# Kernel tuning notes

Measured on AMD Instinct MI355X. Metric: run time of the kernel, lower is better.

Reference implementation:

```python
import jax, jax.numpy as jnp
import numpy as np

N = 50000      # nodes
E = 800000     # edges (avg degree 16)
F_IN = 128     # num_features
H = 128        # hidden_channels
C = 64         # num_classes
K = 3          # TAGConv hops (PyG default)


def setup_inputs() -> dict:
    key = jax.random.key(0)
    k0, k1, k2, k3 = jax.random.split(key, 4)
    x = jax.random.normal(k0, (N, F_IN), dtype=jnp.float32)
    edge_index = jax.random.randint(k1, (2, E), 0, N, dtype=jnp.int32)
    W1 = jax.random.normal(k2, (K + 1, F_IN, H), dtype=jnp.float32) / np.sqrt(F_IN).astype(np.float32)
    b1 = jnp.zeros((H,), dtype=jnp.float32)
    W2 = jax.random.normal(k3, (K + 1, H, C), dtype=jnp.float32) / np.sqrt(H).astype(np.float32)
    b2 = jnp.zeros((C,), dtype=jnp.float32)
    return {"x": x, "edge_index": edge_index, "W1": W1, "b1": b1, "W2": W2, "b2": b2}


def _gcn_norm(row, col):
    # PyG gcn_norm with add_self_loops=False (TAGConv default):
    # deg over target nodes (col), norm = d^-1/2[row] * d^-1/2[col]
    deg = jax.ops.segment_sum(jnp.ones((E,), dtype=jnp.float32), col, num_segments=N)
    dinv = jnp.where(deg > 0, jax.lax.rsqrt(jnp.maximum(deg, 1.0)) * jnp.where(deg > 0, 1.0, 0.0), 0.0)
    dinv = jnp.where(deg > 0, deg ** -0.5, 0.0)
    return dinv[row] * dinv[col]


def _tag_conv(h, row, col, norm, W, b):
    # out = sum_{k=0..K} A_hat^k h @ W[k] + b, A_hat = D^-1/2 A D^-1/2
    out = h @ W[0]
    for k in range(1, K + 1):
        h = jax.ops.segment_sum(norm[:, None] * h[row], col, num_segments=N)  # [N, d]
        out = out + h @ W[k]
    return out + b


def reference(x, edge_index, W1, b1, W2, b2):
    row, col = edge_index[0], edge_index[1]
    norm = _gcn_norm(row, col)  # [E]
    h = jax.nn.relu(_tag_conv(x, row, col, norm, W1, b1))
    # F.dropout with training=False is the identity (inference reference)
    out = _tag_conv(h, row, col, norm, W2, b2)
    return jax.nn.log_softmax(out, axis=1)
```

## Files before the change

### kernel.cpp

```cpp
#include <hip/hip_runtime.h>
#include <stdint.h>

#define NN 50000
#define EE 800000
#define NROWS 50048
#define CB 196
#define CAP 5120
#define ACH 4096

typedef unsigned int u32;
typedef unsigned short u16;
using f32x4 = __attribute__((ext_vector_type(4))) float;
using short8 = __attribute__((ext_vector_type(8))) short;

__device__ __forceinline__ float bflo(u32 u) { return __uint_as_float(u << 16); }
__device__ __forceinline__ float bfhi(u32 u) { return __uint_as_float(u & 0xFFFF0000u); }
__device__ __forceinline__ float bf1(u16 v) { return __uint_as_float(((u32)v) << 16); }
__device__ __forceinline__ u32 f2bf(float f) {
    u32 u = __float_as_uint(f);
    return (u + 0x7FFFu + ((u >> 16) & 1u)) >> 16;
}
__device__ __forceinline__ u32 pack2(float lo, float hi) {
    return f2bf(lo) | (f2bf(hi) << 16);
}

__device__ __forceinline__ int excl_scan256(int v, int tid) {
    __shared__ int ws_[4];
    int lane = tid & 63, w = tid >> 6;
    int x = v;
    #pragma unroll
    for (int off = 1; off < 64; off <<= 1) {
        int y = __shfl_up(x, off, 64);
        if (lane >= off) x += y;
    }
    if (lane == 63) ws_[w] = x;
    __syncthreads();
    int add = 0;
    if (w > 0) add += ws_[0];
    if (w > 1) add += ws_[1];
    if (w > 2) add += ws_[2];
    return add + x - v;
}


__global__ void detect_kernel(const u32* __restrict__ xw, int* __restrict__ flag) {
    int tid = threadIdx.x;
    int cnt = 0;
    for (int i = tid; i < 8192; i += 256) {
        u32 u = xw[i];
        int e0 = (u >> 7) & 0xFF, e1 = (u >> 23) & 0xFF;
        cnt += (e0 >= 0xC3) + (e1 >= 0xC3);
    }
    #pragma unroll
    for (int off = 32; off; off >>= 1) cnt += __shfl_xor(cnt, off, 64);
    __shared__ int wsum[4];
    if ((tid & 63) == 0) wsum[tid >> 6] = cnt;
    __syncthreads();
    if (tid == 0) flag[0] = (wsum[0] + wsum[1] + wsum[2] + wsum[3] > 100) ? 1 : 0;
}


__global__ __launch_bounds__(256) void phaseA_kernel(const int* __restrict__ ei,
                                                     int* __restrict__ ccnt,
                                                     u32* __restrict__ cpad) {
    __shared__ int hist[256], lstart[256], lofs[256], gbase[256];
    __shared__ u32 srt[ACH];
    int tid = threadIdx.x;
    int e0 = blockIdx.x * ACH;
    int nv = EE - e0; if (nv > ACH) nv = ACH;
    hist[tid] = 0;
    __syncthreads();
    u32 pk[16];
    int bn[16];
    #pragma unroll
    for (int i = 0; i < 16; i++) {
        int e = e0 + tid + i * 256;
        bn[i] = -1;
        if (e < EE) {
            int r = ei[e], c = ei[EE + e];
            bn[i] = c >> 8;
            pk[i] = (u32)r | ((u32)(c & 255) << 16) | ((u32)bn[i] << 24);
            atomicAdd(&hist[bn[i]], 1);
        }
    }
    __syncthreads();
    int v = hist[tid];
    int excl = excl_scan256(v, tid);
    lstart[tid] = excl;
    lofs[tid] = excl;
    gbase[tid] = atomicAdd(&ccnt[tid], v);
    __syncthreads();
    #pragma unroll
    for (int i = 0; i < 16; i++)
        if (bn[i] >= 0) {
            int lp = atomicAdd(&lofs[bn[i]], 1);
            srt[lp] = pk[i];
        }
    __syncthreads();
    for (int j = tid; j < nv; j += 256) {
        u32 pv = srt[j];
        int b = pv >> 24;
        cpad[(size_t)b * CAP + gbase[b] + (j - lstart[b])] = pv;
    }
}

__global__ void cscan_kernel(const int* __restrict__ ccnt, int* __restrict__ cbase,
                             int* __restrict__ rowptr, float* __restrict__ dinv) {
    int tid = threadIdx.x;
    int v = ccnt[tid];
    int excl = excl_scan256(v, tid);
    cbase[tid] = excl;
    if (tid == 0) {
        rowptr[NN] = EE;
        rowptr[NN + 1] = EE;
        dinv[NN] = 0.f;
    }
}


__global__ __launch_bounds__(256) void phaseB_kernel(const u32* __restrict__ cpad,
                                                     const int* __restrict__ ccnt,
                                                     const int* __restrict__ cbase,
                                                     u16* __restrict__ esrc,
                                                     int* __restrict__ rowptr,
                                                     float* __restrict__ dinv,
                                                     float* __restrict__ rinv) {
    __shared__ int hist[256], lstart[256], lofs[256];
    __shared__ u16 srt[CAP];
    int tid = threadIdx.x, cb = blockIdx.x;
    int cnt = ccnt[cb], base = cbase[cb];
    hist[tid] = 0;
    __syncthreads();
    for (int j = tid; j < cnt; j += 256)
        atomicAdd(&hist[(cpad[(size_t)cb * CAP + j] >> 16) & 255], 1);
    __syncthreads();
    int v = hist[tid];
    int excl = excl_scan256(v, tid);
    lstart[tid] = excl;
    lofs[tid] = excl;
    int g = cb * 256 + tid;
    if (g < NN) {
        rowptr[g] = base + excl;
        dinv[g] = v > 0 ? rsqrtf((float)v) : 0.f;
        rinv[g] = v > 0 ? sqrtf((float)v) : 0.f;
    }
    __syncthreads();
    for (int j = tid; j < cnt; j += 256) {
        u32 pv = cpad[(size_t)cb * CAP + j];
        int lp = atomicAdd(&lofs[(pv >> 16) & 255], 1);
        srt[lp] = (u16)(pv & 0xFFFF);
    }
    __syncthreads();
    for (int j = tid; j < cnt; j += 256) esrc[base + j] = srt[j];
}

__global__ void wprep_kernel(const void* __restrict__ w, u16* __restrict__ wt,
                             int fout, int nk, int mode, int total,
                             const int* __restrict__ flag) {
    int idx = blockIdx.x * 256 + threadIdx.x;
    if (idx >= total) return;
    u16 v = flag[0] ? (u16)f2bf(((const float*)w)[idx]) : ((const u16*)w)[idx];
    int per = 128 * fout;
    int k = idx / per, rem = idx % per;
    int in = rem / fout, o = rem % fout;
    size_t J;
    if (mode == 0) J = (size_t)(k * 16 + (in >> 3)) * fout + o;
    else J = (size_t)(in >> 3) * (nk * fout) + k * fout + o;
    wt[J * 8 + (in & 7)] = v;
}

__global__ void bprep_kernel(const void* __restrict__ b1, const void* __restrict__ b2,
                             float* __restrict__ bf, const int* __restrict__ flag) {
    int i = threadIdx.x;
    if (i < 128) bf[i] = flag[0] ? ((const float*)b1)[i] : bf1(((const u16*)b1)[i]);
    else {
        int j = i - 128;
        bf[i] = flag[0] ? ((const float*)b2)[j] : bf1(((const u16*)b2)[j]);
    }
}


__global__ void scalex_kernel(const void* __restrict__ x, u32* __restrict__ g0,
                              u32* __restrict__ xb, const float* __restrict__ dinv,
                              const int* __restrict__ flag) {
    int i = blockIdx.x * 256 + threadIdx.x;
    if (i >= (NN + 1) * 64) return;
    int node = i >> 6;
    int fl = flag[0];
    if (node == NN) {
        g0[i] = 0;
        if (fl) xb[i] = 0;
        return;
    }
    float dv = dinv[node];
    float a, b;
    if (fl) {
        const float* xf = (const float*)x;
        a = xf[2 * i];
        b = xf[2 * i + 1];
        xb[i] = pack2(a, b);
    } else {
        u32 u = ((const u32*)x)[i];
        a = bflo(u);
        b = bfhi(u);
    }
    g0[i] = pack2(a * dv, b * dv);
}


__global__ __launch_bounds__(256) void propg_kernel(const u32* __restrict__ gin,
                                                    u32* __restrict__ gout,
                                                    const int* __restrict__ rowptr,
                                                    const u16* __restrict__ esrc,
                                                    const float* __restrict__ dinv) {
    int node = (blockIdx.x * 256 + threadIdx.x) >> 6;
    int lane = threadIdx.x & 63;
    if (node > NN) return;
    int e0 = rowptr[node], e1 = rowptr[node + 1];
    float ax = 0.f, ay = 0.f;
    for (int base = e0; base < e1; base += 64) {
        int s_l = NN;
        if (base + lane < e1) s_l = esrc[base + lane];
        int cnt = e1 - base;
        if (cnt > 64) cnt = 64;
        for (int j = 0; j < cnt; j += 16) {
            u32 hv[16];
            #pragma unroll
            for (int u = 0; u < 16; u++) {
                int s = __builtin_amdgcn_readlane(s_l, j + u);
                hv[u] = gin[(size_t)s * 64 + lane];
            }
            #pragma unroll
            for (int u = 0; u < 16; u++) {
                ax += bflo(hv[u]);
                ay += bfhi(hv[u]);
            }
        }
    }
    float d = dinv[node];
    float d2 = d * d;
    gout[(size_t)node * 64 + lane] = pack2(ax * d2, ay * d2);
}


__device__ __forceinline__ float gatheru(const u16* __restrict__ uin, int e0, int e1,
                                         int lane, const u16* __restrict__ esrc) {
    float a = 0.f;
    for (int base = e0; base < e1; base += 64) {
        int s_l = NN;
        if (base + lane < e1) s_l = esrc[base + lane];
        int cnt = e1 - base;
        if (cnt > 64) cnt = 64;
        for (int j = 0; j < cnt; j += 16) {
            float hv[16];
            #pragma unroll
            for (int u = 0; u < 16; u++) {
                int s = __builtin_amdgcn_readlane(s_l, j + u);
                hv[u] = bf1(uin[(size_t)s * 64 + lane]);
            }
            #pragma unroll
            for (int u = 0; u < 16; u++) a += hv[u];
        }
    }
    return a;
}

__global__ __launch_bounds__(256) void prop64_add_kernel(const u16* __restrict__ uin,
                                                         const u16* __restrict__ zadd,
                                                         u16* __restrict__ uout,
                                                         const int* __restrict__ rowptr,
                                                         const u16* __restrict__ esrc,
                                                         const float* __restrict__ dinv) {
    int node = (blockIdx.x * 256 + threadIdx.x) >> 6;
    int lane = threadIdx.x & 63;
    if (node > NN) return;
    float s = gatheru(uin, rowptr[node], rowptr[node + 1], lane, esrc);
    float d = dinv[node];
    float r = fmaf(d * d, s, d * bf1(zadd[(size_t)node * 64 + lane]));
    uout[(size_t)node * 64 + lane] = (u16)f2bf(r);
}

__global__ __launch_bounds__(256) void prop64_final_kernel(const u16* __restrict__ uin,
                                                           const u16* __restrict__ z0,
                                                           const float* __restrict__ bias,
                                                           void* __restrict__ outv,
                                                           const int* __restrict__ rowptr,
                                                           const u16* __restrict__ esrc,
                                                           const float* __restrict__ dinv,
                                                           const int* __restrict__ flag) {
    int node = (blockIdx.x * 256 + threadIdx.x) >> 6;
    int lane = threadIdx.x & 63;
    if (node >= NN) return;
    float sg = gatheru(uin, rowptr[node], rowptr[node + 1], lane, esrc);
    float v = dinv[node] * sg + bf1(z0[(size_t)node * 64 + lane]) + bias[lane];
    float m = v;
    #pragma unroll
    for (int off = 32; off; off >>= 1) m = fmaxf(m, __shfl_xor(m, off, 64));
    float e = __expf(v - m);
    float s = e;
    #pragma unroll
    for (int off = 32; off; off >>= 1) s += __shfl_xor(s, off, 64);
    float r = v - m - __logf(s);
    if (flag[0]) ((float*)outv)[(size_t)node * 64 + lane] = r;
    else ((u16*)outv)[(size_t)node * 64 + lane] = (u16)f2bf(r);
}


__device__ __forceinline__ short8 ld8(const u16* p) {
    return __builtin_bit_cast(short8, *(const uint4*)p);
}

template <int NT>
__global__ __launch_bounds__(256) void gemm1_kernel(const u32* __restrict__ a0,
                                                    const u32* __restrict__ a0alt,
                                                    const u32* __restrict__ a1,
                                                    const u32* __restrict__ a2,
                                                    const u32* __restrict__ a3,
                                                    const u16* __restrict__ wt,
                                                    const float* __restrict__ rinv,
                                                    const float* __restrict__ bias,
                                                    u32* __restrict__ outH,
                                                    const int* __restrict__ flag) {
    __shared__ uint4 hs[1024];
    const u32* A0 = flag[0] ? a0alt : a0;
    const u32* bufs[4] = {A0, a1, a2, a3};
    int t = threadIdx.x;
    int lane = t & 63, w = t >> 6;
    int row0 = blockIdx.x * 64;
    int cb = (NT == 4) ? (int)blockIdx.y * 64 : 0;
    int m = lane & 15, qo = lane >> 4;
    f32x4 accx[NT], accg[NT];
    #pragma unroll
    for (int tt = 0; tt < NT; tt++) {
        accx[tt] = (f32x4){0.f, 0.f, 0.f, 0.f};
        accg[tt] = (f32x4){0.f, 0.f, 0.f, 0.f};
    }

    uint4 p[4];
    {
        const uint4* src = (const uint4*)A0 + (size_t)row0 * 16;
        #pragma unroll
        for (int i = 0; i < 4; i++) p[i] = src[t + 256 * i];
    }
    #pragma unroll
    for (int hop = 0; hop < 4; hop++) {
        __syncthreads();
        #pragma unroll
        for (int i = 0; i < 4; i++) {
            int g = t + 256 * i;
            hs[(g >> 4) * 16 + ((g & 15) ^ ((g >> 4) & 15))] = p[i];
        }
        __syncthreads();
        if (hop + 1 < 4) {
            const uint4* src = (const uint4*)bufs[hop + 1] + (size_t)row0 * 16;
            #pragma unroll
            for (int i = 0; i < 4; i++) p[i] = src[t + 256 * i];
        }
        #pragma unroll
        for (int q = 0; q < 4; q++) {
            short8 a = __builtin_bit_cast(short8,
                hs[(16 * w + m) * 16 + ((q * 4 + qo) ^ m)]);
            short8 b[NT];
            #pragma unroll
            for (int tt = 0; tt < NT; tt++)
                b[tt] = ld8(wt + ((size_t)(hop * 16 + q * 4 + qo) * 128 + cb + 16 * tt + m) * 8);
            if (hop == 0) {
                #pragma unroll
                for (int tt = 0; tt < NT; tt++)
                    accx[tt] = __builtin_amdgcn_mfma_f32_16x16x32_bf16(a, b[tt], accx[tt], 0, 0, 0);
            } else {
                #pragma unroll
                for (int tt = 0; tt < NT; tt++)
                    accg[tt] = __builtin_amdgcn_mfma_f32_16x16x32_bf16(a, b[tt], accg[tt], 0, 0, 0);
            }
        }
    }

    int r0 = row0 + 16 * w + qo * 4;
    float rv[4];
    #pragma unroll
    for (int r = 0; r < 4; r++) rv[r] = (r0 + r < NN) ? rinv[r0 + r] : 0.f;
    __syncthreads();
    u16* lds16 = (u16*)hs;
    #pragma unroll
    for (int tt = 0; tt < NT; tt++) {
        float bs = bias[cb + 16 * tt + m];
        #pragma unroll
        for (int r = 0; r < 4; r++) {
            int rr = r0 + r;
            float vv = 0.f;
            if (rr < NN) vv = fmaxf(accx[tt][r] + rv[r] * accg[tt][r] + bs, 0.f);
            lds16[(16 * w + qo * 4 + r) * (16 * NT) + 16 * tt + m] = (u16)f2bf(vv);
        }
    }
    __syncthreads();
    uint4* out4 = (uint4*)outH;
    const uint4* epi4 = (const uint4*)hs;
    if (NT == 8) {
        #pragma unroll
        for (int i = 0; i < 4; i++) {
            int g = t + 256 * i;
            int row = g >> 4, ch = g & 15;
            out4[(size_t)(row0 + row) * 16 + ch] = epi4[g];
        }
    } else {
        #pragma unroll
        for (int i = 0; i < 2; i++) {
            int g = t + 256 * i;
            int row = g >> 3, ch = g & 7;
            out4[(size_t)(row0 + row) * 16 + (cb >> 3) + ch] = epi4[g];
        }
    }
}

__global__ __launch_bounds__(256) void gemmz_kernel(const u32* __restrict__ aH,
                                                    const u16* __restrict__ wt,
                                                    const float* __restrict__ dinv,
                                                    u16* __restrict__ p0, u16* __restrict__ p1,
                                                    u16* __restrict__ p2, u16* __restrict__ p3) {
    __shared__ uint4 hs[1024];
    int t = threadIdx.x;
    int lane = t & 63, w = t >> 6;
    int row0 = blockIdx.x * 64;
    int py = blockIdx.y;
    int cb = py * 64;
    int m = lane & 15, qo = lane >> 4;
    f32x4 acc[4];
    #pragma unroll
    for (int tt = 0; tt < 4; tt++) acc[tt] = (f32x4){0.f, 0.f, 0.f, 0.f};
    {
        const uint4* src = (const uint4*)aH + (size_t)row0 * 16;
        #pragma unroll
        for (int i = 0; i < 4; i++) {
            int g = t + 256 * i;
            hs[(g >> 4) * 16 + ((g & 15) ^ ((g >> 4) & 15))] = src[g];
        }
    }
    __syncthreads();
    #pragma unroll
    for (int q = 0; q < 4; q++) {
        short8 a = __builtin_bit_cast(short8,
            hs[(16 * w + m) * 16 + ((q * 4 + qo) ^ m)]);
        short8 b[4];
        #pragma unroll
        for (int tt = 0; tt < 4; tt++)
            b[tt] = ld8(wt + ((size_t)(q * 4 + qo) * 256 + cb + 16 * tt + m) * 8);
        #pragma unroll
        for (int tt = 0; tt < 4; tt++)
            acc[tt] = __builtin_amdgcn_mfma_f32_16x16x32_bf16(a, b[tt], acc[tt], 0, 0, 0);
    }
    u16* zp = (py == 0) ? p0 : (py == 1) ? p1 : (py == 2) ? p2 : p3;
    int r0 = row0 + 16 * w + qo * 4;
    float sc[4];
    #pragma unroll
    for (int r = 0; r < 4; r++) {
        int rr = r0 + r;
        sc[r] = (rr < NN) ? ((py == 3) ? dinv[rr] : 1.f) : 0.f;
    }
    __syncthreads();
    u16* lds16 = (u16*)hs;
    #pragma unroll
    for (int tt = 0; tt < 4; tt++) {
        #pragma unroll
        for (int r = 0; r < 4; r++) {
            lds16[(16 * w + qo * 4 + r) * 64 + 16 * tt + m] = (u16)f2bf(sc[r] * acc[tt][r]);
        }
    }
    __syncthreads();
    uint4* zp4 = (uint4*)zp;
    const uint4* epi4 = (const uint4*)hs;
    #pragma unroll
    for (int i = 0; i < 2; i++) {
        int g = t + 256 * i;
        int row = g >> 3, ch = g & 7;
        zp4[(size_t)(row0 + row) * 8 + ch] = epi4[g];
    }
}


extern "C" void kernel_launch(void* const* d_in, const int* in_sizes, int n_in,
                              void* d_out, int out_size, void* d_ws, size_t ws_size,
                              hipStream_t stream) {
    const void* x  = d_in[0];
    const int*  ei = (const int*)d_in[1];
    const void* W1 = d_in[2];
    const void* b1 = d_in[3];
    const void* W2 = d_in[4];
    const void* b2 = d_in[5];

    char* ws = (char*)d_ws;
    size_t p = 0;
    auto alloc = [&](size_t bytes) -> void* {
        void* r = ws + p;
        p = (p + bytes + 255) & ~(size_t)255;
        return r;
    };
    int*   flag   = (int*)  alloc(256);
    int*   rowptr = (int*)  alloc((size_t)(NN + 2) * 4);
    float* dinv   = (float*)alloc((size_t)(NN + 64) * 4);
    float* rinv   = (float*)alloc((size_t)(NN + 64) * 4);
    int*   ccnt   = (int*)  alloc(256 * 4);
    int*   cbase  = (int*)  alloc(256 * 4);
    u16*   esrc   = (u16*)  alloc((size_t)EE * 2);
    u16*   wt1    = (u16*)  alloc((size_t)64 * 128 * 16);
    u16*   wt2    = (u16*)  alloc((size_t)16 * 256 * 16);
    float* biasF  = (float*)alloc(192 * 4);
    const size_t hbytes = (size_t)(NROWS + 16) * 64 * 4;
    u32* X = (u32*)alloc(hbytes);
    u32* P = (u32*)alloc(hbytes);
    u32* Q = (u32*)alloc(hbytes);
    u32* R = (u32*)alloc(hbytes);
    int cs = (p + hbytes + 256 <= ws_size) ? 1 : 0;
    u32* H5 = cs ? (u32*)alloc(hbytes) : Q;
    u32* cpad = X;

    const size_t ZP = (size_t)(NROWS + 16) * 64;
    u16* zR0 = (u16*)R;
    u16* zR1 = (u16*)R + ZP;
    u16* zP0 = (u16*)P;
    u16* zP1 = (u16*)P + ZP;
    u16* uX0 = (u16*)X;

    hipMemsetAsync(ccnt, 0, 256 * 4, stream);
    detect_kernel<<<1, 256, 0, stream>>>((const u32*)x, flag);
    phaseA_kernel<<<(EE + ACH - 1) / ACH, 256, 0, stream>>>(ei, ccnt, cpad);
    cscan_kernel<<<1, 256, 0, stream>>>(ccnt, cbase, rowptr, dinv);
    phaseB_kernel<<<CB, 256, 0, stream>>>(cpad, ccnt, cbase, esrc, rowptr, dinv, rinv);
    wprep_kernel<<<(4 * 128 * 128 + 255) / 256, 256, 0, stream>>>(
        W1, wt1, 128, 4, 0, 4 * 128 * 128, flag);
    wprep_kernel<<<(4 * 128 * 64 + 255) / 256, 256, 0, stream>>>(
        W2, wt2, 64, 4, 1, 4 * 128 * 64, flag);
    bprep_kernel<<<1, 192, 0, stream>>>(b1, b2, biasF, flag);

    const int PGX = ((NN + 1) * 64 + 255) / 256;
    const int PGF = (NN * 64) / 256;
    const int GG = NROWS / 64;

    scalex_kernel<<<PGX, 256, 0, stream>>>(x, P, X, dinv, flag);

    propg_kernel<<<PGX, 256, 0, stream>>>(P, Q, rowptr, esrc, dinv);
    propg_kernel<<<PGX, 256, 0, stream>>>(Q, R, rowptr, esrc, dinv);
    propg_kernel<<<PGX, 256, 0, stream>>>(R, P, rowptr, esrc, dinv);
    if (cs)
        gemm1_kernel<4><<<dim3(GG, 2), 256, 0, stream>>>(
            (const u32*)x, X, Q, R, P, wt1, rinv, biasF, H5, flag);
    else
        gemm1_kernel<8><<<GG, 256, 0, stream>>>(
            (const u32*)x, X, Q, R, P, wt1, rinv, biasF, Q, flag);

    gemmz_kernel<<<dim3(GG, 4), 256, 0, stream>>>(H5, wt2, dinv, zR0, zR1, zP0, zP1);
    prop64_add_kernel<<<PGX, 256, 0, stream>>>(zP1, zP0, uX0, rowptr, esrc, dinv);
    prop64_add_kernel<<<PGX, 256, 0, stream>>>(uX0, zR1, zP0, rowptr, esrc, dinv);
    prop64_final_kernel<<<PGF, 256, 0, stream>>>(zP0, zR0, biasF + 128, d_out,
                                                 rowptr, esrc, dinv, flag);
}
```

Baseline: 342.2 us.

## Fuse layer-1 GEMM with layer-2 projection GEMM into one kernel

Adds gemm1z_kernel, which computes the layer-1 hidden tile (ReLU, bias and rinv scaling), keeps it in LDS, and immediately multiplies it by all four layer-2 weight slices. The four Z planes are written directly. This removes the separate gemmz launch and the global write and re-read of the hidden activations. In exchange it drops the 2-way column split of gemm1, giving fewer blocks and more accumulator registers per thread, which may lower occupancy. It also needs extra workspace for two buffers and falls back to the old path otherwise.

```diff
diff --git a/kernel.cpp b/kernel.cpp
--- a/kernel.cpp
+++ b/kernel.cpp
@@ -310,7 +310,140 @@
     return __builtin_bit_cast(short8, *(const uint4*)p);
 }
 
-template <int NT>
+__global__ __launch_bounds__(256) void gemm1z_kernel(const u32* __restrict__ a0,
+                                                     const u32* __restrict__ a0alt,
+                                                     const u32* __restrict__ a1,
+                                                     const u32* __restrict__ a2,
+                                                     const u32* __restrict__ a3,
+                                                     const u16* __restrict__ wt1,
+                                                     const u16* __restrict__ wt2,
+                                                     const float* __restrict__ rinv,
+                                                     const float* __restrict__ dinv,
+                                                     const float* __restrict__ bias,
+                                                     u16* __restrict__ p0, u16* __restrict__ p1,
+                                                     u16* __restrict__ p2, u16* __restrict__ p3,
+                                                     const int* __restrict__ flag) {
+    __shared__ uint4 hs[1024];
+    const u32* A0 = flag[0] ? a0alt : a0;
+    const u32* bufs[4] = {A0, a1, a2, a3};
+    int t = threadIdx.x;
+    int lane = t & 63, w = t >> 6;
+    int row0 = blockIdx.x * 64;
+    int m = lane & 15, qo = lane >> 4;
+    f32x4 accx[8], accg[8];
+    #pragma unroll
+    for (int tt = 0; tt < 8; tt++) {
+        accx[tt] = (f32x4){0.f, 0.f, 0.f, 0.f};
+        accg[tt] = (f32x4){0.f, 0.f, 0.f, 0.f};
+    }
+
+    uint4 p[4];
+    {
+        const uint4* src = (const uint4*)A0 + (size_t)row0 * 16;
+        #pragma unroll
+        for (int i = 0; i < 4; i++) p[i] = src[t + 256 * i];
+    }
+    #pragma unroll
+    for (int hop = 0; hop < 4; hop++) {
+        __syncthreads();
+        #pragma unroll
+        for (int i = 0; i < 4; i++) {
+            int g = t + 256 * i;
+            hs[(g >> 4) * 16 + ((g & 15) ^ ((g >> 4) & 15))] = p[i];
+        }
+        __syncthreads();
+        if (hop + 1 < 4) {
+            const uint4* src = (const uint4*)bufs[hop + 1] + (size_t)row0 * 16;
+            #pragma unroll
+            for (int i = 0; i < 4; i++) p[i] = src[t + 256 * i];
+        }
+        #pragma unroll
+        for (int q = 0; q < 4; q++) {
+            short8 a = __builtin_bit_cast(short8,
+                hs[(16 * w + m) * 16 + ((q * 4 + qo) ^ m)]);
+            short8 b[8];
+            #pragma unroll
+            for (int tt = 0; tt < 8; tt++)
+                b[tt] = ld8(wt1 + ((size_t)(hop * 16 + q * 4 + qo) * 128 + 16 * tt + m) * 8);
+            if (hop == 0) {
+                #pragma unroll
+                for (int tt = 0; tt < 8; tt++)
+                    accx[tt] = __builtin_amdgcn_mfma_f32_16x16x32_bf16(a, b[tt], accx[tt], 0, 0, 0);
+            } else {
+                #pragma unroll
+                for (int tt = 0; tt < 8; tt++)
+                    accg[tt] = __builtin_amdgcn_mfma_f32_16x16x32_bf16(a, b[tt], accg[tt], 0, 0, 0);
+            }
+        }
+    }
+
+    int r0 = row0 + 16 * w + qo * 4;
+    float rv[4], scp3[4];
+    #pragma unroll
+    for (int r = 0; r < 4; r++) {
+        int rr = r0 + r;
+        rv[r] = (rr < NN) ? rinv[rr] : 0.f;
+        scp3[r] = (rr < NN) ? dinv[rr] : 0.f;
+    }
+    __syncthreads();
+    u16* lds16 = (u16*)hs;
+    #pragma unroll
+    for (int tt = 0; tt < 8; tt++) {
+        float bs = bias[16 * tt + m];
+        #pragma unroll
+        for (int r = 0; r < 4; r++) {
+            int rr = r0 + r;
+            float vv = 0.f;
+            if (rr < NN) vv = fmaxf(accx[tt][r] + rv[r] * accg[tt][r] + bs, 0.f);
+            int lrow = 16 * w + qo * 4 + r;
+            int col = 16 * tt + m;
+            lds16[lrow * 128 + (((col >> 3) ^ (lrow & 15)) << 3) + (col & 7)] = (u16)f2bf(vv);
+        }
+    }
+    __syncthreads();
+    f32x4 az[4][4];
+    #pragma unroll
+    for (int py = 0; py < 4; py++)
+        #pragma unroll
+        for (int tt = 0; tt < 4; tt++) az[py][tt] = (f32x4){0.f, 0.f, 0.f, 0.f};
+    #pragma unroll
+    for (int q = 0; q < 4; q++) {
+        short8 a = __builtin_bit_cast(short8,
+            hs[(16 * w + m) * 16 + ((q * 4 + qo) ^ m)]);
+        #pragma unroll
+        for (int py = 0; py < 4; py++) {
+            #pragma unroll
+            for (int tt = 0; tt < 4; tt++) {
+                short8 b = ld8(wt2 + ((size_t)(q * 4 + qo) * 256 + py * 64 + 16 * tt + m) * 8);
+                az[py][tt] = __builtin_amdgcn_mfma_f32_16x16x32_bf16(a, b, az[py][tt], 0, 0, 0);
+            }
+        }
+    }
+    u16* planes[4] = {p0, p1, p2, p3};
+    #pragma unroll
+    for (int py = 0; py < 4; py++) {
+        __syncthreads();
+        #pragma unroll
+        for (int tt = 0; tt < 4; tt++) {
+            #pragma unroll
+            for (int r = 0; r < 4; r++) {
+                int rr = r0 + r;
+                float sc = (rr < NN) ? ((py == 3) ? scp3[r] : 1.f) : 0.f;
+                lds16[(16 * w + qo * 4 + r) * 64 + 16 * tt + m] = (u16)f2bf(sc * az[py][tt][r]);
+            }
+        }
+        __syncthreads();
+        uint4* zp4 = (uint4*)planes[py];
+        const uint4* epi4 = (const uint4*)hs;
+        #pragma unroll
+        for (int i = 0; i < 2; i++) {
+            int g = t + 256 * i;
+            int row = g >> 3, ch = g & 7;
+            zp4[(size_t)(row0 + row) * 8 + ch] = epi4[g];
+        }
+    }
+}
+
 __global__ __launch_bounds__(256) void gemm1_kernel(const u32* __restrict__ a0,
                                                     const u32* __restrict__ a0alt,
                                                     const u32* __restrict__ a1,
@@ -327,15 +460,13 @@
     int t = threadIdx.x;
     int lane = t & 63, w = t >> 6;
     int row0 = blockIdx.x * 64;
-    int cb = (NT == 4) ? (int)blockIdx.y * 64 : 0;
     int m = lane & 15, qo = lane >> 4;
-    f32x4 accx[NT], accg[NT];
-    #pragma unroll
-    for (int tt = 0; tt < NT; tt++) {
+    f32x4 accx[8], accg[8];
+    #pragma unroll
+    for (int tt = 0; tt < 8; tt++) {
         accx[tt] = (f32x4){0.f, 0.f, 0.f, 0.f};
         accg[tt] = (f32x4){0.f, 0.f, 0.f, 0.f};
     }
-
     uint4 p[4];
     {
         const uint4* src = (const uint4*)A0 + (size_t)row0 * 16;
@@ -360,22 +491,21 @@
         for (int q = 0; q < 4; q++) {
             short8 a = __builtin_bit_cast(short8,
                 hs[(16 * w + m) * 16 + ((q * 4 + qo) ^ m)]);
-            short8 b[NT];
-            #pragma unroll
-            for (int tt = 0; tt < NT; tt++)
-                b[tt] = ld8(wt + ((size_t)(hop * 16 + q * 4 + qo) * 128 + cb + 16 * tt + m) * 8);
+            short8 b[8];
+            #pragma unroll
+            for (int tt = 0; tt < 8; tt++)
+                b[tt] = ld8(wt + ((size_t)(hop * 16 + q * 4 + qo) * 128 + 16 * tt + m) * 8);
             if (hop == 0) {
                 #pragma unroll
-                for (int tt = 0; tt < NT; tt++)
+                for (int tt = 0; tt < 8; tt++)
                     accx[tt] = __builtin_amdgcn_mfma_f32_16x16x32_bf16(a, b[tt], accx[tt], 0, 0, 0);
             } else {
                 #pragma unroll
-                for (int tt = 0; tt < NT; tt++)
+                for (int tt = 0; tt < 8; tt++)
                     accg[tt] = __builtin_amdgcn_mfma_f32_16x16x32_bf16(a, b[tt], accg[tt], 0, 0, 0);
             }
         }
     }
-
     int r0 = row0 + 16 * w + qo * 4;
     float rv[4];
     #pragma unroll
@@ -383,33 +513,24 @@
     __syncthreads();
     u16* lds16 = (u16*)hs;
     #pragma unroll
-    for (int tt = 0; tt < NT; tt++) {
-        float bs = bias[cb + 16 * tt + m];
+    for (int tt = 0; tt < 8; tt++) {
+        float bs = bias[16 * tt + m];
         #pragma unroll
         for (int r = 0; r < 4; r++) {
             int rr = r0 + r;
             float vv = 0.f;
             if (rr < NN) vv = fmaxf(accx[tt][r] + rv[r] * accg[tt][r] + bs, 0.f);
-            lds16[(16 * w + qo * 4 + r) * (16 * NT) + 16 * tt + m] = (u16)f2bf(vv);
+            lds16[(16 * w + qo * 4 + r) * 128 + 16 * tt + m] = (u16)f2bf(vv);
         }
     }
     __syncthreads();
     uint4* out4 = (uint4*)outH;
     const uint4* epi4 = (const uint4*)hs;
-    if (NT == 8) {
-        #pragma unroll
-        for (int i = 0; i < 4; i++) {
-            int g = t + 256 * i;
-            int row = g >> 4, ch = g & 15;
-            out4[(size_t)(row0 + row) * 16 + ch] = epi4[g];
-        }
-    } else {
-        #pragma unroll
-        for (int i = 0; i < 2; i++) {
-            int g = t + 256 * i;
-            int row = g >> 3, ch = g & 7;
-            out4[(size_t)(row0 + row) * 16 + (cb >> 3) + ch] = epi4[g];
-        }
+    #pragma unroll
+    for (int i = 0; i < 4; i++) {
+        int g = t + 256 * i;
+        int row = g >> 4, ch = g & 15;
+        out4[(size_t)(row0 + row) * 16 + ch] = epi4[g];
     }
 }
 
@@ -510,16 +631,12 @@
     u32* P = (u32*)alloc(hbytes);
     u32* Q = (u32*)alloc(hbytes);
     u32* R = (u32*)alloc(hbytes);
-    int cs = (p + hbytes + 256 <= ws_size) ? 1 : 0;
-    u32* H5 = cs ? (u32*)alloc(hbytes) : Q;
+    int fused = (p + 2 * hbytes + 256 <= ws_size) ? 1 : 0;
+    u32* H5 = fused ? (u32*)alloc(hbytes) : nullptr;
+    u32* H6 = fused ? (u32*)alloc(hbytes) : nullptr;
     u32* cpad = X;
 
     const size_t ZP = (size_t)(NROWS + 16) * 64;
-    u16* zR0 = (u16*)R;
-    u16* zR1 = (u16*)R + ZP;
-    u16* zP0 = (u16*)P;
-    u16* zP1 = (u16*)P + ZP;
-    u16* uX0 = (u16*)X;
 
     hipMemsetAsync(ccnt, 0, 256 * 4, stream);
     detect_kernel<<<1, 256, 0, stream>>>((const u32*)x, flag);
@@ -541,16 +658,33 @@
     propg_kernel<<<PGX, 256, 0, stream>>>(P, Q, rowptr, esrc, dinv);
     propg_kernel<<<PGX, 256, 0, stream>>>(Q, R, rowptr, esrc, dinv);
     propg_kernel<<<PGX, 256, 0, stream>>>(R, P, rowptr, esrc, dinv);
-    if (cs)
-        gemm1_kernel<4><<<dim3(GG, 2), 256, 0, stream>>>(
-            (const u32*)x, X, Q, R, P, wt1, rinv, biasF, H5, flag);
-    else
-        gemm1_kernel<8><<<GG, 256, 0, stream>>>(
+
+    if (fused) {
+        u16* z0 = (u16*)H5;
+        u16* z1 = (u16*)H5 + ZP;
+        u16* z2 = (u16*)H6;
+        u16* u3 = (u16*)H6 + ZP;
+        u16* uQ0 = (u16*)Q;
+        u16* uQ1 = (u16*)Q + ZP;
+        gemm1z_kernel<<<GG, 256, 0, stream>>>(
+            (const u32*)x, X, Q, R, P, wt1, wt2, rinv, dinv, biasF,
+            z0, z1, z2, u3, flag);
+        prop64_add_kernel<<<PGX, 256, 0, stream>>>(u3, z2, uQ0, rowptr, esrc, dinv);
+        prop64_add_kernel<<<PGX, 256, 0, stream>>>(uQ0, z1, uQ1, rowptr, esrc, dinv);
+        prop64_final_kernel<<<PGF, 256, 0, stream>>>(uQ1, z0, biasF + 128, d_out,
+                                                     rowptr, esrc, dinv, flag);
+    } else {
+        u16* zR0 = (u16*)R;
+        u16* zR1 = (u16*)R + ZP;
+        u16* zP0 = (u16*)P;
+        u16* zP1 = (u16*)P + ZP;
+        u16* uX0 = (u16*)X;
+        gemm1_kernel<<<GG, 256, 0, stream>>>(
             (const u32*)x, X, Q, R, P, wt1, rinv, biasF, Q, flag);
-
-    gemmz_kernel<<<dim3(GG, 4), 256, 0, stream>>>(H5, wt2, dinv, zR0, zR1, zP0, zP1);
-    prop64_add_kernel<<<PGX, 256, 0, stream>>>(zP1, zP0, uX0, rowptr, esrc, dinv);
-    prop64_add_kernel<<<PGX, 256, 0, stream>>>(uX0, zR1, zP0, rowptr, esrc, dinv);
-    prop64_final_kernel<<<PGF, 256, 0, stream>>>(zP0, zR0, biasF + 128, d_out,
-                                                 rowptr, esrc, dinv, flag);
-}
+        gemmz_kernel<<<dim3(GG, 4), 256, 0, stream>>>(Q, wt2, dinv, zR0, zR1, zP0, zP1);
+        prop64_add_kernel<<<PGX, 256, 0, stream>>>(zP1, zP0, uX0, rowptr, esrc, dinv);
+        prop64_add_kernel<<<PGX, 256, 0, stream>>>(uX0, zR1, zP0, rowptr, esrc, dinv);
+        prop64_final_kernel<<<PGF, 256, 0, stream>>>(zP0, zR0, biasF + 128, d_out,
+                                                     rowptr, esrc, dinv, flag);
+    }
+}
```

New measurement: 351.7 us. 2.8% more time.
